# Optimization experiments

Hardware: AMD Instinct MI355X
Metric: run time of the kernel (lower is better)

## Reference

```python
import jax, jax.numpy as jnp
import numpy as np

B, S, E, H = 2, 2048, 1024, 16
DH = E // H  # 64
EPS = 1e-5


def layer_norm(x, g, b):
    mu = jnp.mean(x, axis=-1, keepdims=True)
    var = jnp.mean(jnp.square(x - mu), axis=-1, keepdims=True)
    return (x - mu) * jax.lax.rsqrt(var + EPS) * g + b


def setup_inputs() -> dict:
    key = jax.random.key(0)
    ks = jax.random.split(key, 12)
    s = lambda fan_in: 1.0 / np.sqrt(fan_in)
    return {
        "x": jax.random.normal(ks[0], (B, S, E), dtype=jnp.float32),
        "ln1_g": jnp.ones((E,), jnp.float32),
        "ln1_b": jnp.zeros((E,), jnp.float32),
        # per-head projections, batched over head axis: [H, E, DH]
        "Wq": jax.random.uniform(ks[1], (H, E, DH), jnp.float32, -s(E), s(E)),
        "Wk": jax.random.uniform(ks[2], (H, E, DH), jnp.float32, -s(E), s(E)),
        "Wv": jax.random.uniform(ks[3], (H, E, DH), jnp.float32, -s(E), s(E)),
        "Wo": jax.random.uniform(ks[4], (H * DH, E), jnp.float32, -s(H * DH), s(H * DH)),
        "bo": jax.random.uniform(ks[5], (E,), jnp.float32, -s(H * DH), s(H * DH)),
        "ln2_g": jnp.ones((E,), jnp.float32),
        "ln2_b": jnp.zeros((E,), jnp.float32),
        "W1": jax.random.uniform(ks[6], (E, 4 * E), jnp.float32, -s(E), s(E)),
        "b1": jax.random.uniform(ks[7], (4 * E,), jnp.float32, -s(E), s(E)),
        "W2": jax.random.uniform(ks[8], (4 * E, E), jnp.float32, -s(4 * E), s(4 * E)),
        "b2": jax.random.uniform(ks[9], (E,), jnp.float32, -s(4 * E), s(4 * E)),
    }


def reference(x, ln1_g, ln1_b, Wq, Wk, Wv, Wo, bo, ln2_g, ln2_b, W1, b1, W2, b2):
    b, s, e = x.shape
    # --- multi-head attention (pre-LN) ---
    h = layer_norm(x, ln1_g, ln1_b)
    q = jnp.einsum("bse,hed->bhsd", h, Wq)
    k = jnp.einsum("bse,hed->bhsd", h, Wk)
    v = jnp.einsum("bse,hed->bhsd", h, Wv)
    # NOTE: original scales by channel**-0.5 (embed_size), not head_size
    scores = jnp.einsum("bhsd,bhtd->bhst", q, k) * (e ** -0.5)
    causal = jnp.tril(jnp.ones((s, s), dtype=bool))
    scores = jnp.where(causal, scores, -jnp.inf)
    attn = jax.nn.softmax(scores, axis=-1)  # dropout is identity in eval
    out = jnp.einsum("bhst,bhtd->bhsd", attn, v)
    out = out.transpose(0, 2, 1, 3).reshape(b, s, -1)  # concat heads: [B,S,H*DH]
    x = x + out @ Wo + bo
    # --- feed-forward (pre-LN) ---
    h2 = layer_norm(x, ln2_g, ln2_b)
    ff = jax.nn.relu(h2 @ W1 + b1) @ W2 + b2
    return x + ff
```

## Files before the change

### kernel.cpp

```cpp
#include <hip/hip_runtime.h>


typedef __bf16 bf16_t;
typedef __attribute__((ext_vector_type(8))) __bf16 bf16x8;
typedef __attribute__((ext_vector_type(4))) __bf16 bf16x4;
typedef __attribute__((ext_vector_type(4))) float f32x4;

#define B_DIM 2
#define S_DIM 2048
#define E_DIM 1024
#define H_DIM 16
#define DH_DIM 64

#define GLD16(gp, lp) __builtin_amdgcn_global_load_lds( \
    (const __attribute__((address_space(1))) void*)(gp), \
    (__attribute__((address_space(3))) void*)(lp), 16, 0, 0)

#define Q_SCALE 0.0450842120f

__global__ __launch_bounds__(256) void ln_kernel(
    const float* __restrict__ x, const float* __restrict__ g,
    const float* __restrict__ bv, bf16_t* __restrict__ out)
{
  const int row = blockIdx.x;
  const int t = threadIdx.x;
  const float* xr = x + (size_t)row * E_DIM;
  float4 v = *(const float4*)&xr[t * 4];
  float s  = v.x + v.y + v.z + v.w;
  float s2 = v.x*v.x + v.y*v.y + v.z*v.z + v.w*v.w;
#pragma unroll
  for (int m = 1; m < 64; m <<= 1) {
    s  += __shfl_xor(s,  m, 64);
    s2 += __shfl_xor(s2, m, 64);
  }
  __shared__ float red[8];
  const int wid = t >> 6, lane = t & 63;
  if (lane == 0) { red[wid] = s; red[4 + wid] = s2; }
  __syncthreads();
  s  = red[0] + red[1] + red[2] + red[3];
  s2 = red[4] + red[5] + red[6] + red[7];
  const float mu  = s * (1.f / E_DIM);
  const float var = s2 * (1.f / E_DIM) - mu * mu;
  const float rs  = rsqrtf(var + 1e-5f);
  float4 gg = *(const float4*)&g[t * 4];
  float4 bb = *(const float4*)&bv[t * 4];
  bf16x4 o;
  o[0] = (bf16_t)((v.x - mu) * rs * gg.x + bb.x);
  o[1] = (bf16_t)((v.y - mu) * rs * gg.y + bb.y);
  o[2] = (bf16_t)((v.z - mu) * rs * gg.z + bb.z);
  o[3] = (bf16_t)((v.w - mu) * rs * gg.w + bb.w);
  *(bf16x4*)&out[(size_t)row * E_DIM + t * 4] = o;
}

__global__ __launch_bounds__(256) void transpose_cast(
    const float* __restrict__ src, bf16_t* __restrict__ dst, int R, int C)
{
  __shared__ float tile[64][65];
  const int c0 = blockIdx.x * 64, r0 = blockIdx.y * 64;
  const int t = threadIdx.x;
  const int rr = t >> 2;
#pragma unroll
  for (int u = 0; u < 4; u++) {
    const int cc = (t & 3) * 4 + u * 16;
    float4 f = *(const float4*)&src[(size_t)(r0 + rr) * C + c0 + cc];
    tile[rr][cc + 0] = f.x; tile[rr][cc + 1] = f.y;
    tile[rr][cc + 2] = f.z; tile[rr][cc + 3] = f.w;
  }
  __syncthreads();
  const int oc = t >> 2;
#pragma unroll
  for (int u = 0; u < 4; u++) {
    const int orr = (t & 3) * 4 + u * 16;
    bf16x4 w;
    w[0] = (bf16_t)tile[orr + 0][oc];
    w[1] = (bf16_t)tile[orr + 1][oc];
    w[2] = (bf16_t)tile[orr + 2][oc];
    w[3] = (bf16_t)tile[orr + 3][oc];
    *(bf16x4*)&dst[(size_t)(c0 + oc) * R + r0 + orr] = w;
  }
}

__global__ __launch_bounds__(256) void qkv_transpose(
    const float* __restrict__ Wq, const float* __restrict__ Wk,
    const float* __restrict__ Wv, bf16_t* __restrict__ dstT)
{
  const int m = blockIdx.y >> 4, h = blockIdx.y & 15;
  const float* src = (m == 0 ? Wq : (m == 1 ? Wk : Wv)) + (size_t)h * E_DIM * DH_DIM;
  const int e0 = blockIdx.x * 64;
  __shared__ float tile[64][65];
  const int t = threadIdx.x;
  const int rr = t >> 2;
#pragma unroll
  for (int u = 0; u < 4; u++) {
    const int cc = (t & 3) * 4 + u * 16;
    float4 f = *(const float4*)&src[(size_t)(e0 + rr) * DH_DIM + cc];
    tile[rr][cc + 0] = f.x; tile[rr][cc + 1] = f.y;
    tile[rr][cc + 2] = f.z; tile[rr][cc + 3] = f.w;
  }
  __syncthreads();
  const int oc = t >> 2;
  const size_t drow = (size_t)(m * 1024 + h * 64 + oc) * E_DIM;
#pragma unroll
  for (int u = 0; u < 4; u++) {
    const int orr = (t & 3) * 4 + u * 16;
    bf16x4 w;
    w[0] = (bf16_t)tile[orr + 0][oc];
    w[1] = (bf16_t)tile[orr + 1][oc];
    w[2] = (bf16_t)tile[orr + 2][oc];
    w[3] = (bf16_t)tile[orr + 3][oc];
    *(bf16x4*)&dstT[drow + e0 + orr] = w;
  }
}

constexpr int EPI_QKV = 0, EPI_BIAS_RES = 1, EPI_BIAS_RELU = 2;

template <int EPI>
__global__ __launch_bounds__(256) void gemm_kernel(
    const bf16_t* __restrict__ A, const bf16_t* __restrict__ Bt,
    int M, int N, int K,
    const float* __restrict__ bias, const float* __restrict__ resid,
    float* __restrict__ outF, bf16_t* __restrict__ outB,
    bf16_t* __restrict__ qo, bf16_t* __restrict__ ko, bf16_t* __restrict__ vo)
{
  __shared__ bf16_t As[128 * 32];
  __shared__ bf16_t Bs[128 * 32];
  const int gx = gridDim.x;
  const int nwg = gx * gridDim.y;
  int id = blockIdx.y * gx + blockIdx.x;
  id = (id & 7) * (nwg >> 3) + (id >> 3);
  const int m0 = (id % gx) * 128, n0 = (id / gx) * 128;

  const int tid = threadIdx.x, lane = tid & 63, wid = tid >> 6;
  const int wr = wid >> 1, wc = wid & 1;
  const int lr = lane & 15, lg = lane >> 4;
  const int rl = lane >> 2, k8 = (lane & 3) * 8;

  const f32x4 z4 = {0.f, 0.f, 0.f, 0.f};
  f32x4 acc[4][4];
#pragma unroll
  for (int i = 0; i < 4; i++)
#pragma unroll
    for (int j = 0; j < 4; j++) acc[i][j] = z4;

  for (int k0 = 0; k0 < K; k0 += 32) {
    __syncthreads();
#pragma unroll
    for (int q = 0; q < 2; q++) {
      const int row = q * 64 + wid * 16 + rl;
      GLD16(A  + (size_t)(m0 + row) * K + k0 + k8, &As[(q * 64 + wid * 16) * 32]);
      GLD16(Bt + (size_t)(n0 + row) * K + k0 + k8, &Bs[(q * 64 + wid * 16) * 32]);
    }
    __syncthreads();
    bf16x8 af[4], bfr[4];
#pragma unroll
    for (int i = 0; i < 4; i++)
      af[i]  = *(const bf16x8*)&As[(wr * 64 + i * 16 + lr) * 32 + lg * 8];
#pragma unroll
    for (int j = 0; j < 4; j++)
      bfr[j] = *(const bf16x8*)&Bs[(wc * 64 + j * 16 + lr) * 32 + lg * 8];
    __builtin_amdgcn_s_setprio(1);
#pragma unroll
    for (int i = 0; i < 4; i++)
#pragma unroll
      for (int j = 0; j < 4; j++)
        acc[i][j] = __builtin_amdgcn_mfma_f32_16x16x32_bf16(af[i], bfr[j], acc[i][j], 0, 0, 0);
    __builtin_amdgcn_s_setprio(0);
  }

#pragma unroll
  for (int i = 0; i < 4; i++) {
#pragma unroll
    for (int j = 0; j < 4; j++) {
#pragma unroll
      for (int r = 0; r < 4; r++) {
        const int m = m0 + wr * 64 + i * 16 + lg * 4 + r;
        const int n = n0 + wc * 64 + j * 16 + lr;
        const float val = acc[i][j][r];
        if constexpr (EPI == EPI_QKV) {
          const int tsel = n >> 10, h = (n >> 6) & 15, d = n & 63;
          const int b = m >> 11, s = m & 2047;
          const size_t idx = ((size_t)((b * H_DIM + h) * S_DIM + s)) * DH_DIM + d;
          if (tsel == 0)      qo[idx] = (bf16_t)(val * Q_SCALE);
          else if (tsel == 1) ko[idx] = (bf16_t)val;
          else                vo[idx] = (bf16_t)val;
        } else if constexpr (EPI == EPI_BIAS_RES) {
          outF[(size_t)m * N + n] = val + bias[n] + resid[(size_t)m * N + n];
        } else {
          const float u = val + bias[n];
          outB[(size_t)m * N + n] = (bf16_t)(u > 0.f ? u : 0.f);
        }
      }
    }
  }
}

__global__ __launch_bounds__(256) void attn_kernel(
    const bf16_t* __restrict__ Q, const bf16_t* __restrict__ K,
    const bf16_t* __restrict__ V, bf16_t* __restrict__ O,
    bf16_t* __restrict__ Opart, float* __restrict__ mpart, float* __restrict__ lpart)
{
  __shared__ bf16_t Ks[2][64 * 64];
  __shared__ bf16_t Vst[2][64 * 64];
  __shared__ bf16_t Ps[4][16 * 64];

  const int nwg = 80 * gridDim.y;
  int id = blockIdx.y * 80 + blockIdx.x;
  id = (id & 7) * (nwg >> 3) + (id >> 3);
  const int bx = id % 80, bh = id / 80;

  int qt, sp, ns;
  if (bx < 8)       { qt = bx;                sp = 0;            ns = 1; }
  else if (bx < 24) { qt = 8 + ((bx - 8) >> 1);  sp = (bx - 8) & 1;  ns = 2; }
  else if (bx < 48) { const int u = bx - 24; const int q3 = u / 3;
                      qt = 16 + q3;           sp = u - q3 * 3;   ns = 3; }
  else              { const int u = bx - 48;  qt = 24 + (u >> 2); sp = u & 3; ns = 4; }
  const int n = qt + 1;
  const int lo = (sp * n) / ns, hi = ((sp + 1) * n) / ns;

  const int q0b = qt * 64;
  const int tid = threadIdx.x;
  const int wid = tid >> 6, lane = tid & 63;
  const int lr = lane & 15, lg = lane >> 4;
  const int q0w = q0b + wid * 16;

  const bf16_t* Qp = Q + (size_t)bh * S_DIM * DH_DIM;
  const bf16_t* Kp = K + (size_t)bh * S_DIM * DH_DIM;
  const bf16_t* Vp = V + (size_t)bh * S_DIM * DH_DIM;

  bf16x8 bq[2];
#pragma unroll
  for (int c = 0; c < 2; c++)
    bq[c] = *(const bf16x8*)&Qp[(size_t)(q0w + lr) * DH_DIM + c * 32 + lg * 8];

  const f32x4 z4 = {0.f, 0.f, 0.f, 0.f};
  f32x4 Ot[4];
#pragma unroll
  for (int dt = 0; dt < 4; dt++) Ot[dt] = z4;
  float mrow = -1e30f, lrow = 0.f;

  const int st = tid >> 3;
  const int s8 = tid & 7;
  const int sbl = lane & 48;
  const int ktr = wid * 8 + (lane >> 3);
  const int ksc = (lane & 7);

  {
    const int t0 = lo * 64;
#pragma unroll
    for (int p = 0; p < 2; p++) {
      const int tr = p * 32 + ktr;
      GLD16(Kp + (size_t)(t0 + tr) * DH_DIM + (ksc ^ (tr & 7)) * 8,
            &Ks[0][(p * 32 + wid * 8) * 64]);
    }
  }
  bf16x8 vc0 = *(const bf16x8*)&Vp[(size_t)(lo * 64 + st) * DH_DIM + s8 * 8];
  bf16x8 vc1 = *(const bf16x8*)&Vp[(size_t)(lo * 64 + 32 + st) * DH_DIM + s8 * 8];
  bf16x8 vn0 = vc0, vn1 = vc1;

  for (int tc = lo; tc < hi; ++tc) {
    const int cur = (tc - lo) & 1;
#pragma unroll
    for (int h2 = 0; h2 < 2; h2++) {
      const bf16x8 vv = h2 ? vc1 : vc0;
      const int t = h2 * 32 + st;
#pragma unroll
      for (int j = 0; j < 8; j++) {
        const int d = s8 * 8 + j;
        const int f = j ^ s8;
        Vst[cur][(d * 128 + ((t * 2) ^ (f << 4))) >> 1] = vv[j];
      }
    }
    __syncthreads();
    if (tc + 1 < hi) {
      const int t1 = (tc + 1) * 64;
#pragma unroll
      for (int p = 0; p < 2; p++) {
        const int tr = p * 32 + ktr;
        GLD16(Kp + (size_t)(t1 + tr) * DH_DIM + (ksc ^ (tr & 7)) * 8,
              &Ks[cur ^ 1][(p * 32 + wid * 8) * 64]);
      }
      vn0 = *(const bf16x8*)&Vp[(size_t)(t1 + st) * DH_DIM + s8 * 8];
      vn1 = *(const bf16x8*)&Vp[(size_t)(t1 + 32 + st) * DH_DIM + s8 * 8];
    }

    const int t0 = tc * 64;
    f32x4 sc[4];
    __builtin_amdgcn_s_setprio(1);
#pragma unroll
    for (int j = 0; j < 4; j++) {
      f32x4 s = z4;
      const int t = j * 16 + lr;
#pragma unroll
      for (int c = 0; c < 2; c++) {
        const int kbyte = t * 128 + (((c * 4 + lg) * 16) ^ ((t & 7) << 4));
        bf16x8 ak = *(const bf16x8*)((const char*)&Ks[cur][0] + kbyte);
        s = __builtin_amdgcn_mfma_f32_16x16x32_bf16(ak, bq[c], s, 0, 0, 0);
      }
      sc[j] = s;
    }
    __builtin_amdgcn_s_setprio(0);
    if (tc == qt) {
#pragma unroll
      for (int j = 0; j < 4; j++)
#pragma unroll
        for (int r = 0; r < 4; r++) {
          const int tg = t0 + j * 16 + lg * 4 + r;
          if (tg > q0w + lr) sc[j][r] = -1e30f;
        }
    }
    float tmax = sc[0][0];
#pragma unroll
    for (int j = 0; j < 4; j++)
#pragma unroll
      for (int r = 0; r < 4; r++) tmax = fmaxf(tmax, sc[j][r]);
    tmax = fmaxf(tmax, __shfl_xor(tmax, 16, 64));
    tmax = fmaxf(tmax, __shfl_xor(tmax, 32, 64));
    const float mnew = fmaxf(mrow, tmax);
    const float fsc = __builtin_exp2f(mrow - mnew);
    mrow = mnew;
    float tsum = 0.f;
#pragma unroll
    for (int j = 0; j < 4; j++)
#pragma unroll
      for (int r = 0; r < 4; r++) {
        const float p = __builtin_exp2f(sc[j][r] - mnew);
        sc[j][r] = p;
        tsum += p;
      }
    tsum += __shfl_xor(tsum, 16, 64);
    tsum += __shfl_xor(tsum, 32, 64);
    lrow = lrow * fsc + tsum;

#pragma unroll
    for (int j = 0; j < 4; j++) {
      bf16x4 w;
#pragma unroll
      for (int r = 0; r < 4; r++) w[r] = (bf16_t)sc[j][r];
      const int pbyte = lr * 128 + ((j * 32 + lg * 8) ^ ((lr & 7) << 4));
      *(bf16x4*)((char*)&Ps[wid][0] + pbyte) = w;
    }
    float fr[4];
#pragma unroll
    for (int r = 0; r < 4; r++) fr[r] = __shfl(fsc, sbl | (lg * 4 + r), 64);
#pragma unroll
    for (int dt = 0; dt < 4; dt++)
#pragma unroll
      for (int r = 0; r < 4; r++) Ot[dt][r] *= fr[r];
    __builtin_amdgcn_s_setprio(1);
#pragma unroll
    for (int c = 0; c < 2; c++) {
      const int abyte = lr * 128 + ((c * 64 + lg * 16) ^ ((lr & 7) << 4));
      bf16x8 pa = *(const bf16x8*)((const char*)&Ps[wid][0] + abyte);
#pragma unroll
      for (int dt = 0; dt < 4; dt++) {
        const int d = dt * 16 + lr;
        const int f = (d & 7) ^ ((d >> 3) & 7);
        const int vbyte = d * 128 + (((c * 4 + lg) * 16) ^ (f << 4));
        bf16x8 bv = *(const bf16x8*)((const char*)&Vst[cur][0] + vbyte);
        Ot[dt] = __builtin_amdgcn_mfma_f32_16x16x32_bf16(pa, bv, Ot[dt], 0, 0, 0);
      }
    }
    __builtin_amdgcn_s_setprio(0);
    vc0 = vn0; vc1 = vn1;
  }

  if (ns == 1) {
    float linv[4];
#pragma unroll
    for (int r = 0; r < 4; r++)
      linv[r] = 1.f / __shfl(lrow, sbl | (lg * 4 + r), 64);
    const int b = bh >> 4, h = bh & 15;
#pragma unroll
    for (int r = 0; r < 4; r++) {
      const int s = q0w + lg * 4 + r;
      const size_t base = ((size_t)(b * S_DIM + s)) * E_DIM + h * DH_DIM;
#pragma unroll
      for (int dt = 0; dt < 4; dt++)
        O[base + dt * 16 + lr] = (bf16_t)(Ot[dt][r] * linv[r]);
    }
  } else {
    const int sbase = (qt < 16) ? 8 + 2 * (qt - 8)
                     : (qt < 24) ? 24 + 3 * (qt - 16) : 48 + 4 * (qt - 24);
    const int slot = bh * 80 + sbase + sp;
    bf16_t* Ob = Opart + (size_t)slot * 64 * 64;
#pragma unroll
    for (int r = 0; r < 4; r++)
#pragma unroll
      for (int dt = 0; dt < 4; dt++)
        Ob[(wid * 16 + lg * 4 + r) * 64 + dt * 16 + lr] = (bf16_t)Ot[dt][r];
    if (lg == 0) {
      mpart[slot * 64 + wid * 16 + lr] = mrow;
      lpart[slot * 64 + wid * 16 + lr] = lrow;
    }
  }
}

__global__ __launch_bounds__(256) void attn_combine(
    const bf16_t* __restrict__ Opart, const float* __restrict__ mpart,
    const float* __restrict__ lpart, bf16_t* __restrict__ O)
{
  const int qt = 8 + blockIdx.x;
  const int bh = blockIdx.y;
  const int ns = (qt < 16) ? 2 : (qt < 24) ? 3 : 4;
  const int sbase = (qt < 16) ? 8 + 2 * (qt - 8)
                   : (qt < 24) ? 24 + 3 * (qt - 16) : 48 + 4 * (qt - 24);
  const int slot0 = bh * 80 + sbase;
  const int tid = threadIdx.x;
  const int q = tid >> 2, d0 = (tid & 3) * 16;

  float M = -1e30f;
  for (int s = 0; s < ns; s++) M = fmaxf(M, mpart[(slot0 + s) * 64 + q]);
  float L = 0.f;
  float acc[16];
#pragma unroll
  for (int j = 0; j < 16; j++) acc[j] = 0.f;
  for (int s = 0; s < ns; s++) {
    const float w = __builtin_exp2f(mpart[(slot0 + s) * 64 + q] - M);
    L += w * lpart[(slot0 + s) * 64 + q];
    const bf16_t* Ob = Opart + ((size_t)(slot0 + s) * 64 + q) * 64 + d0;
    bf16x8 o0 = *(const bf16x8*)Ob;
    bf16x8 o1 = *(const bf16x8*)(Ob + 8);
#pragma unroll
    for (int j = 0; j < 8; j++) { acc[j] += w * (float)o0[j]; acc[8 + j] += w * (float)o1[j]; }
  }
  const float inv = 1.f / L;
  const int b = bh >> 4, h = bh & 15;
  const int srow = qt * 64 + q;
  bf16_t* out = O + ((size_t)(b * S_DIM + srow)) * E_DIM + h * DH_DIM + d0;
  bf16x8 w0, w1;
#pragma unroll
  for (int j = 0; j < 8; j++) { w0[j] = (bf16_t)(acc[j] * inv); w1[j] = (bf16_t)(acc[8 + j] * inv); }
  *(bf16x8*)out = w0;
  *(bf16x8*)(out + 8) = w1;
}

extern "C" void kernel_launch(void* const* d_in, const int* in_sizes, int n_in,
                              void* d_out, int out_size, void* d_ws, size_t ws_size,
                              hipStream_t stream)
{
  const float* x    = (const float*)d_in[0];
  const float* ln1g = (const float*)d_in[1];
  const float* ln1b = (const float*)d_in[2];
  const float* Wq   = (const float*)d_in[3];
  const float* Wk   = (const float*)d_in[4];
  const float* Wv   = (const float*)d_in[5];
  const float* Wo   = (const float*)d_in[6];
  const float* bo   = (const float*)d_in[7];
  const float* ln2g = (const float*)d_in[8];
  const float* ln2b = (const float*)d_in[9];
  const float* W1   = (const float*)d_in[10];
  const float* b1   = (const float*)d_in[11];
  const float* W2   = (const float*)d_in[12];
  const float* b2   = (const float*)d_in[13];

  char* ws = (char*)d_ws;
  bf16_t* WqkvT = (bf16_t*)(ws + 0);
  bf16_t* WoT   = (bf16_t*)(ws + 6291456);
  bf16_t* W1T   = (bf16_t*)(ws + 8388608);
  bf16_t* W2T   = (bf16_t*)(ws + 16777216);
  bf16_t* h1    = (bf16_t*)(ws + 25165824);
  bf16_t* qb    = (bf16_t*)(ws + 33554432);
  bf16_t* kb    = (bf16_t*)(ws + 41943040);
  bf16_t* vb    = (bf16_t*)(ws + 50331648);
  bf16_t* attnb = (bf16_t*)(ws + 58720256);
  float*  xmid  = (float* )(ws + 67108864);
  bf16_t* h2    = (bf16_t*)(ws + 83886080);
  bf16_t* ff1   = (bf16_t*)(ws + 25165824);
  bf16_t* Opart = (bf16_t*)(ws + 67108864);
  float*  mpart = (float* )(ws + 25165824);
  float*  lpart = (float* )(ws + 25821184);

  qkv_transpose<<<dim3(16, 48), 256, 0, stream>>>(Wq, Wk, Wv, WqkvT);
  transpose_cast<<<dim3(16, 16), 256, 0, stream>>>(Wo, WoT, 1024, 1024);
  transpose_cast<<<dim3(64, 16), 256, 0, stream>>>(W1, W1T, 1024, 4096);
  transpose_cast<<<dim3(16, 64), 256, 0, stream>>>(W2, W2T, 4096, 1024);

  ln_kernel<<<4096, 256, 0, stream>>>(x, ln1g, ln1b, h1);
  gemm_kernel<EPI_QKV><<<dim3(32, 24), 256, 0, stream>>>(
      h1, WqkvT, 4096, 3072, 1024, nullptr, nullptr, nullptr, nullptr, qb, kb, vb);
  attn_kernel<<<dim3(80, 32), 256, 0, stream>>>(qb, kb, vb, attnb, Opart, mpart, lpart);
  attn_combine<<<dim3(24, 32), 256, 0, stream>>>(Opart, mpart, lpart, attnb);
  gemm_kernel<EPI_BIAS_RES><<<dim3(32, 8), 256, 0, stream>>>(
      attnb, WoT, 4096, 1024, 1024, bo, x, xmid, nullptr, nullptr, nullptr, nullptr);
  ln_kernel<<<4096, 256, 0, stream>>>(xmid, ln2g, ln2b, h2);
  gemm_kernel<EPI_BIAS_RELU><<<dim3(32, 32), 256, 0, stream>>>(
      h2, W1T, 4096, 4096, 1024, b1, nullptr, nullptr, ff1, nullptr, nullptr, nullptr);
  gemm_kernel<EPI_BIAS_RES><<<dim3(32, 8), 256, 0, stream>>>(
      ff1, W2T, 4096, 1024, 4096, b2, xmid, (float*)d_out, nullptr, nullptr, nullptr, nullptr);

  (void)in_sizes; (void)n_in; (void)out_size; (void)ws_size;
}
```

Measured before the change: 294.9 us.

## Split-K the N=1024 GEMMs, double-buffer GEMM LDS, fuse reduction with LN2

The two output-projection GEMMs (Wo and W2) are split along K into 2 and 4 slices, raising the workgroup count from 256 to 512 and 1024 so the CUs are better filled. Partial sums are written to workspace: fp32 for Wo, bf16 for W2. New reduce kernels sum the partials and add bias and residual. The Wo reduce is fused with the second LayerNorm, which removes the separate LN pass. The GEMM main loop also gains double-buffered LDS with one barrier per K step, so the next tile's global-to-LDS loads overlap the current MFMAs. The cost is extra partial-sum memory traffic and reduced precision from the bf16 partials.

```diff
diff --git a/kernel.cpp b/kernel.cpp
--- a/kernel.cpp
+++ b/kernel.cpp
@@ -52,6 +52,73 @@
   *(bf16x4*)&out[(size_t)row * E_DIM + t * 4] = o;
 }
 
+__global__ __launch_bounds__(256) void reduce2_ln(
+    const float* __restrict__ p, const float* __restrict__ bo,
+    const float* __restrict__ x, const float* __restrict__ g,
+    const float* __restrict__ bv, float* __restrict__ xmid, bf16_t* __restrict__ h2)
+{
+  const int row = blockIdx.x;
+  const int t = threadIdx.x;
+  const size_t off = (size_t)row * E_DIM + t * 4;
+  float4 a  = *(const float4*)&p[off];
+  float4 b4 = *(const float4*)&p[(size_t)4096 * E_DIM + off];
+  float4 xr = *(const float4*)&x[off];
+  float4 bo4 = *(const float4*)&bo[t * 4];
+  float4 v;
+  v.x = a.x + b4.x + xr.x + bo4.x;
+  v.y = a.y + b4.y + xr.y + bo4.y;
+  v.z = a.z + b4.z + xr.z + bo4.z;
+  v.w = a.w + b4.w + xr.w + bo4.w;
+  *(float4*)&xmid[off] = v;
+  float s  = v.x + v.y + v.z + v.w;
+  float s2 = v.x*v.x + v.y*v.y + v.z*v.z + v.w*v.w;
+#pragma unroll
+  for (int m = 1; m < 64; m <<= 1) {
+    s  += __shfl_xor(s,  m, 64);
+    s2 += __shfl_xor(s2, m, 64);
+  }
+  __shared__ float red[8];
+  const int wid = t >> 6, lane = t & 63;
+  if (lane == 0) { red[wid] = s; red[4 + wid] = s2; }
+  __syncthreads();
+  s  = red[0] + red[1] + red[2] + red[3];
+  s2 = red[4] + red[5] + red[6] + red[7];
+  const float mu  = s * (1.f / E_DIM);
+  const float var = s2 * (1.f / E_DIM) - mu * mu;
+  const float rs  = rsqrtf(var + 1e-5f);
+  float4 gg = *(const float4*)&g[t * 4];
+  float4 bb = *(const float4*)&bv[t * 4];
+  bf16x4 o;
+  o[0] = (bf16_t)((v.x - mu) * rs * gg.x + bb.x);
+  o[1] = (bf16_t)((v.y - mu) * rs * gg.y + bb.y);
+  o[2] = (bf16_t)((v.z - mu) * rs * gg.z + bb.z);
+  o[3] = (bf16_t)((v.w - mu) * rs * gg.w + bb.w);
+  *(bf16x4*)&h2[off] = o;
+}
+
+__global__ __launch_bounds__(256) void reduce4(
+    const bf16_t* __restrict__ p0, const bf16_t* __restrict__ p1,
+    const bf16_t* __restrict__ p2, const bf16_t* __restrict__ p3,
+    const float* __restrict__ b2, const float* __restrict__ xm,
+    float* __restrict__ out)
+{
+  const int row = blockIdx.x;
+  const int t = threadIdx.x;
+  const size_t off = (size_t)row * E_DIM + t * 4;
+  bf16x4 a0 = *(const bf16x4*)&p0[off];
+  bf16x4 a1 = *(const bf16x4*)&p1[off];
+  bf16x4 a2 = *(const bf16x4*)&p2[off];
+  bf16x4 a3 = *(const bf16x4*)&p3[off];
+  float4 xr = *(const float4*)&xm[off];
+  float4 bb = *(const float4*)&b2[t * 4];
+  float4 o;
+  o.x = (float)a0[0] + (float)a1[0] + (float)a2[0] + (float)a3[0] + xr.x + bb.x;
+  o.y = (float)a0[1] + (float)a1[1] + (float)a2[1] + (float)a3[1] + xr.y + bb.y;
+  o.z = (float)a0[2] + (float)a1[2] + (float)a2[2] + (float)a3[2] + xr.z + bb.z;
+  o.w = (float)a0[3] + (float)a1[3] + (float)a2[3] + (float)a3[3] + xr.w + bb.w;
+  *(float4*)&out[off] = o;
+}
+
 __global__ __launch_bounds__(256) void transpose_cast(
     const float* __restrict__ src, bf16_t* __restrict__ dst, int R, int C)
 {
@@ -112,29 +179,41 @@
   }
 }
 
-constexpr int EPI_QKV = 0, EPI_BIAS_RES = 1, EPI_BIAS_RELU = 2;
+constexpr int EPI_QKV = 0, EPI_BIAS_RELU = 2, EPI_PART_F32 = 3, EPI_PART_B16 = 4;
 
 template <int EPI>
 __global__ __launch_bounds__(256) void gemm_kernel(
     const bf16_t* __restrict__ A, const bf16_t* __restrict__ Bt,
-    int M, int N, int K,
+    int M, int N, int Kst, int Klen,
     const float* __restrict__ bias, const float* __restrict__ resid,
     float* __restrict__ outF, bf16_t* __restrict__ outB,
     bf16_t* __restrict__ qo, bf16_t* __restrict__ ko, bf16_t* __restrict__ vo)
 {
-  __shared__ bf16_t As[128 * 32];
-  __shared__ bf16_t Bs[128 * 32];
+  __shared__ bf16_t As[2][128 * 32];
+  __shared__ bf16_t Bs[2][128 * 32];
   const int gx = gridDim.x;
   const int nwg = gx * gridDim.y;
   int id = blockIdx.y * gx + blockIdx.x;
   id = (id & 7) * (nwg >> 3) + (id >> 3);
   const int m0 = (id % gx) * 128, n0 = (id / gx) * 128;
+  const int sp = blockIdx.z;
+  A  += (size_t)sp * Klen;
+  Bt += (size_t)sp * Klen;
 
   const int tid = threadIdx.x, lane = tid & 63, wid = tid >> 6;
   const int wr = wid >> 1, wc = wid & 1;
   const int lr = lane & 15, lg = lane >> 4;
   const int rl = lane >> 2, k8 = (lane & 3) * 8;
 
+  auto stage = [&](int buf, int k0) {
+#pragma unroll
+    for (int q = 0; q < 2; q++) {
+      const int row = q * 64 + wid * 16 + rl;
+      GLD16(A  + (size_t)(m0 + row) * Kst + k0 + k8, &As[buf][(q * 64 + wid * 16) * 32]);
+      GLD16(Bt + (size_t)(n0 + row) * Kst + k0 + k8, &Bs[buf][(q * 64 + wid * 16) * 32]);
+    }
+  };
+
   const f32x4 z4 = {0.f, 0.f, 0.f, 0.f};
   f32x4 acc[4][4];
 #pragma unroll
@@ -142,22 +221,19 @@
 #pragma unroll
     for (int j = 0; j < 4; j++) acc[i][j] = z4;
 
-  for (int k0 = 0; k0 < K; k0 += 32) {
+  const int nt = Klen / 32;
+  stage(0, 0);
+  for (int it = 0; it < nt; ++it) {
+    const int cur = it & 1;
     __syncthreads();
-#pragma unroll
-    for (int q = 0; q < 2; q++) {
-      const int row = q * 64 + wid * 16 + rl;
-      GLD16(A  + (size_t)(m0 + row) * K + k0 + k8, &As[(q * 64 + wid * 16) * 32]);
-      GLD16(Bt + (size_t)(n0 + row) * K + k0 + k8, &Bs[(q * 64 + wid * 16) * 32]);
-    }
-    __syncthreads();
+    if (it + 1 < nt) stage(cur ^ 1, (it + 1) * 32);
     bf16x8 af[4], bfr[4];
 #pragma unroll
     for (int i = 0; i < 4; i++)
-      af[i]  = *(const bf16x8*)&As[(wr * 64 + i * 16 + lr) * 32 + lg * 8];
+      af[i]  = *(const bf16x8*)&As[cur][(wr * 64 + i * 16 + lr) * 32 + lg * 8];
 #pragma unroll
     for (int j = 0; j < 4; j++)
-      bfr[j] = *(const bf16x8*)&Bs[(wc * 64 + j * 16 + lr) * 32 + lg * 8];
+      bfr[j] = *(const bf16x8*)&Bs[cur][(wc * 64 + j * 16 + lr) * 32 + lg * 8];
     __builtin_amdgcn_s_setprio(1);
 #pragma unroll
     for (int i = 0; i < 4; i++)
@@ -183,11 +259,14 @@
           if (tsel == 0)      qo[idx] = (bf16_t)(val * Q_SCALE);
           else if (tsel == 1) ko[idx] = (bf16_t)val;
           else                vo[idx] = (bf16_t)val;
-        } else if constexpr (EPI == EPI_BIAS_RES) {
-          outF[(size_t)m * N + n] = val + bias[n] + resid[(size_t)m * N + n];
-        } else {
+        } else if constexpr (EPI == EPI_BIAS_RELU) {
           const float u = val + bias[n];
           outB[(size_t)m * N + n] = (bf16_t)(u > 0.f ? u : 0.f);
+        } else if constexpr (EPI == EPI_PART_F32) {
+          outF[(size_t)sp * M * N + (size_t)m * N + n] = val;
+        } else {
+          bf16_t* o = sp == 0 ? outB : sp == 1 ? qo : sp == 2 ? ko : vo;
+          o[(size_t)m * N + n] = (bf16_t)val;
         }
       }
     }
@@ -469,6 +548,11 @@
   bf16_t* Opart = (bf16_t*)(ws + 67108864);
   float*  mpart = (float* )(ws + 25165824);
   float*  lpart = (float* )(ws + 25821184);
+  float*  po    = (float* )(ws + 25165824);
+  bf16_t* pf0   = (bf16_t*)(ws + 0);
+  bf16_t* pf1   = (bf16_t*)(ws + 8388608);
+  bf16_t* pf2   = (bf16_t*)(ws + 58720256);
+  bf16_t* pf3   = (bf16_t*)(ws + 83886080);
 
   qkv_transpose<<<dim3(16, 48), 256, 0, stream>>>(Wq, Wk, Wv, WqkvT);
   transpose_cast<<<dim3(16, 16), 256, 0, stream>>>(Wo, WoT, 1024, 1024);
@@ -476,17 +560,22 @@
   transpose_cast<<<dim3(16, 64), 256, 0, stream>>>(W2, W2T, 4096, 1024);
 
   ln_kernel<<<4096, 256, 0, stream>>>(x, ln1g, ln1b, h1);
-  gemm_kernel<EPI_QKV><<<dim3(32, 24), 256, 0, stream>>>(
-      h1, WqkvT, 4096, 3072, 1024, nullptr, nullptr, nullptr, nullptr, qb, kb, vb);
+  gemm_kernel<EPI_QKV><<<dim3(32, 24, 1), 256, 0, stream>>>(
+      h1, WqkvT, 4096, 3072, 1024, 1024, nullptr, nullptr,
+      nullptr, nullptr, qb, kb, vb);
   attn_kernel<<<dim3(80, 32), 256, 0, stream>>>(qb, kb, vb, attnb, Opart, mpart, lpart);
   attn_combine<<<dim3(24, 32), 256, 0, stream>>>(Opart, mpart, lpart, attnb);
-  gemm_kernel<EPI_BIAS_RES><<<dim3(32, 8), 256, 0, stream>>>(
-      attnb, WoT, 4096, 1024, 1024, bo, x, xmid, nullptr, nullptr, nullptr, nullptr);
-  ln_kernel<<<4096, 256, 0, stream>>>(xmid, ln2g, ln2b, h2);
-  gemm_kernel<EPI_BIAS_RELU><<<dim3(32, 32), 256, 0, stream>>>(
-      h2, W1T, 4096, 4096, 1024, b1, nullptr, nullptr, ff1, nullptr, nullptr, nullptr);
-  gemm_kernel<EPI_BIAS_RES><<<dim3(32, 8), 256, 0, stream>>>(
-      ff1, W2T, 4096, 1024, 4096, b2, xmid, (float*)d_out, nullptr, nullptr, nullptr, nullptr);
+  gemm_kernel<EPI_PART_F32><<<dim3(32, 8, 2), 256, 0, stream>>>(
+      attnb, WoT, 4096, 1024, 1024, 512, nullptr, nullptr,
+      po, nullptr, nullptr, nullptr, nullptr);
+  reduce2_ln<<<4096, 256, 0, stream>>>(po, bo, x, ln2g, ln2b, xmid, h2);
+  gemm_kernel<EPI_BIAS_RELU><<<dim3(32, 32, 1), 256, 0, stream>>>(
+      h2, W1T, 4096, 4096, 1024, 1024, b1, nullptr,
+      nullptr, ff1, nullptr, nullptr, nullptr);
+  gemm_kernel<EPI_PART_B16><<<dim3(32, 8, 4), 256, 0, stream>>>(
+      ff1, W2T, 4096, 1024, 4096, 1024, nullptr, nullptr,
+      nullptr, pf0, pf1, pf2, pf3);
+  reduce4<<<4096, 256, 0, stream>>>(pf0, pf1, pf2, pf3, b2, xmid, (float*)d_out);
 
   (void)in_sizes; (void)n_in; (void)out_size; (void)ws_size;
 }
```

New measurement: 284.9 us. -3.4%, faster.
